# Performance work log

Measured on AMD Instinct MI355X. Metric: run time of the kernel, lower is better.

Reference implementation:

```python
import jax, jax.numpy as jnp
import numpy as np

NU, NI, DU, DI, E, B, T = 100000, 50000, 256, 256, 128, 8192, 24

def setup_inputs() -> dict:
    key = jax.random.key(0)
    ks = jax.random.split(key, 12)
    s = 0.05
    return {
        "nodes": jax.random.randint(ks[0], (B,), 0, NU),
        "neigh_idx": jax.random.randint(ks[1], (B, T), 0, NI),
        "u_weight": jax.random.normal(ks[2], (NU, DU), jnp.float32),
        "i_weight": jax.random.normal(ks[3], (NI, DI), jnp.float32),
        "uW": jax.random.normal(ks[4], (DU, E), jnp.float32) * s,
        "ub": jnp.zeros((E,), jnp.float32),
        "iW": jax.random.normal(ks[5], (DI, E), jnp.float32) * s,
        "ib": jnp.zeros((E,), jnp.float32),
        "aW1": jax.random.normal(ks[6], (2 * E, E), jnp.float32) * s,
        "ab1": jnp.zeros((E,), jnp.float32),
        "aW2": jax.random.normal(ks[7], (E, E), jnp.float32) * s,
        "ab2": jnp.zeros((E,), jnp.float32),
        "aW3": jax.random.normal(ks[8], (E, 1), jnp.float32) * s,
        "ab3": jnp.zeros((1,), jnp.float32),
    }


def reference(nodes, neigh_idx, u_weight, i_weight, uW, ub, iW, ib,
              aW1, ab1, aW2, ab2, aW3, ab3):
    # node features: u_layer(ufeature.weight[nodes])  -> [B, E]
    nodes_fea = u_weight[nodes] @ uW + ub
    # neighbor features: i_layer(ifeature.weight[interactions]) -> [B, T, E]
    neighs = i_weight[neigh_idx] @ iW + ib
    # attention MLP over cat(neigh_feat, node_feat.repeat) -> softmax over T
    x = jnp.concatenate(
        [neighs, jnp.broadcast_to(nodes_fea[:, None, :], neighs.shape)], axis=-1)
    h = jax.nn.relu(x @ aW1 + ab1)
    h = jax.nn.relu(h @ aW2 + ab2)
    logits = (h @ aW3 + ab3)[..., 0]            # [B, T]
    att = jax.nn.softmax(logits, axis=-1)       # softmax over neighbors (dim=0 per node)
    # attention-weighted aggregation: neighs_feature.T @ att_w  -> [B, E]
    agg = jnp.einsum('bt,bte->be', att, neighs)
    # scatter into embed_matrix rows of the batch nodes
    embed_matrix = jnp.zeros((NU, E), jnp.float32).at[nodes].set(agg)
    return nodes_fea, embed_matrix
```

## Files before the change

kernel.cpp:

```cpp
#include <hip/hip_runtime.h>
#include <math.h>

#define NU 100000
#define NI 50000
#define DK 256
#define EN 128
#define BB 8192
#define TT 24

typedef short short8 __attribute__((ext_vector_type(8)));
typedef float f32x4  __attribute__((ext_vector_type(4)));

#define WPACK_SHORTS 114688
#define WP_OFF     0
#define OWNER_OFF  229376
#define NTAB_OFF   629376
#define NPART_OFF  13429376

#define OFF_IWT   0
#define OFF_UWT   32768
#define OFF_AW1UT 65536
#define OFF_AW1LT 81920
#define OFF_AW2T  98304

#define NBLK_NEIGH 782
#define NBLK_NF    128
#define NBLK_PACK  448
#define GGA 4
#define ATTN_BLKS  (BB / GGA)

__device__ __forceinline__ unsigned short f2b(float x) {
    unsigned int u = __float_as_uint(x);
    u = (u + 0x7FFFu + ((u >> 16) & 1u)) >> 16;
    return (unsigned short)u;
}
__device__ __forceinline__ float b2f(unsigned short v) {
    return __uint_as_float(((unsigned int)v) << 16);
}
__device__ __forceinline__ unsigned int cvtpk_bf16(float lo, float hi) {
    unsigned int r;
    asm("v_cvt_pk_bf16_f32 %0, %1, %2" : "=v"(r) : "v"(lo), "v"(hi));
    return r;
}

#define MFMA(a, b, c) __builtin_amdgcn_mfma_f32_16x16x32_bf16((a), (b), (c), 0, 0, 0)
#define LDROW(buf, stride, row, k) \
    (*reinterpret_cast<const short8*>(reinterpret_cast<const char*>(buf) + (row) * (stride) + (k) * 2))

__global__ __launch_bounds__(256)
void prep_kernel(const int* __restrict__ nodes,
                 const float* __restrict__ uW, const float* __restrict__ iW,
                 const float* __restrict__ aW1, const float* __restrict__ aW2,
                 short* __restrict__ wp, int* __restrict__ owner)
{
    if (blockIdx.x < NBLK_PACK) {
        int i = blockIdx.x * 256 + threadIdx.x;
        float v;
        if (i < 32768)      { int j = i;         int n = j >> 8, k = j & 255; v = iW[k * EN + n]; }
        else if (i < 65536) { int j = i - 32768; int n = j >> 8, k = j & 255; v = uW[k * EN + n]; }
        else if (i < 81920) { int j = i - 65536; int n = j >> 7, k = j & 127; v = aW1[k * EN + n]; }
        else if (i < 98304) { int j = i - 81920; int n = j >> 7, k = j & 127; v = aW1[(128 + k) * EN + n]; }
        else                { int j = i - 98304; int n = j >> 7, k = j & 127; v = aW2[k * EN + n]; }
        wp[i] = (short)f2b(v);
    } else {
        int b = (blockIdx.x - NBLK_PACK) * 256 + threadIdx.x;
        if (b < BB) owner[nodes[b]] = -1;
    }
}

__global__ __launch_bounds__(256, 4)
void embed_kernel(const int* __restrict__ nodes,
                  const float* __restrict__ u_weight, const float* __restrict__ i_weight,
                  const float* __restrict__ ub, const float* __restrict__ ib,
                  const float* __restrict__ ab1,
                  const short* __restrict__ wp, int* __restrict__ owner,
                  short* __restrict__ ntab, float* __restrict__ out_nf,
                  float* __restrict__ npart, float* __restrict__ out_embed)
{
    __shared__ __align__(16) char smem[33792];
    __shared__ int sNd[64];

    const int tid = threadIdx.x;
    const int l = tid & 63, lr = l & 15, lq = l >> 4, n0 = (tid >> 6) * 32;
    const int kA = lq * 8, nc0 = n0 + lr, nc1 = n0 + 16 + lr;

    if (blockIdx.x < NBLK_NEIGH) {
        const int r0 = blockIdx.x * 64;
        const int nrows = (NI - r0 < 64) ? (NI - r0) : 64;

        for (int task = tid; task < 64 * 32; task += 256) {
            int row = task >> 5, c = task & 31;
            if (row < nrows) {
                const float* src = i_weight + (size_t)(r0 + row) * DK + c * 8;
                float4 f0 = *(const float4*)src;
                float4 f1 = *(const float4*)(src + 4);
                short8 o;
                o[0]=f2b(f0.x); o[1]=f2b(f0.y); o[2]=f2b(f0.z); o[3]=f2b(f0.w);
                o[4]=f2b(f1.x); o[5]=f2b(f1.y); o[6]=f2b(f1.z); o[7]=f2b(f1.w);
                *reinterpret_cast<short8*>(smem + row * 528 + c * 16) = o;
            }
        }
        __syncthreads();

        const short* iWt = wp + OFF_IWT;
        f32x4 acc[4][2];
        #pragma unroll
        for (int m = 0; m < 4; ++m) { acc[m][0] = {0.f,0.f,0.f,0.f}; acc[m][1] = {0.f,0.f,0.f,0.f}; }
        #pragma unroll
        for (int ks = 0; ks < 8; ++ks) {
            int k = ks * 32 + kA;
            short8 w0 = *reinterpret_cast<const short8*>(iWt + nc0 * DK + k);
            short8 w1 = *reinterpret_cast<const short8*>(iWt + nc1 * DK + k);
            #pragma unroll
            for (int m = 0; m < 4; ++m) {
                short8 a = LDROW(smem, 528, m * 16 + lr, k);
                acc[m][0] = MFMA(a, w0, acc[m][0]);
                acc[m][1] = MFMA(a, w1, acc[m][1]);
            }
        }
        __syncthreads();
        {
            float ib0 = ib[nc0], ib1 = ib[nc1];
            #pragma unroll
            for (int m = 0; m < 4; ++m)
                #pragma unroll
                for (int nt = 0; nt < 2; ++nt) {
                    int n = nt ? nc1 : nc0;
                    float bv = nt ? ib1 : ib0;
                    #pragma unroll
                    for (int r = 0; r < 4; ++r) {
                        int row = m * 16 + lq * 4 + r;
                        *reinterpret_cast<short*>(smem + row * 264 + n * 2)
                            = (short)f2b(acc[m][nt][r] + bv);
                    }
                }
        }
        __syncthreads();
        for (int g = tid; g < nrows * 16; g += 256) {
            int row = g >> 4, s = g & 15;
            short8 v = *reinterpret_cast<const short8*>(smem + row * 264 + s * 16);
            *reinterpret_cast<short8*>(ntab + (size_t)(r0 + row) * EN + s * 8) = v;
        }
    } else {
        const int bblk = blockIdx.x - NBLK_NEIGH;
        const int r0 = bblk * 64;
        {
            int bq = bblk * 256 + tid;
            if (bq < BB) atomicMax(&owner[nodes[bq]], bq);
        }
        if (tid < 64) sNd[tid] = nodes[r0 + tid];
        __syncthreads();

        for (int task = tid; task < 64 * 32; task += 256) {
            int row = task >> 5, c = task & 31;
            const float* src = u_weight + (size_t)sNd[row] * DK + c * 8;
            float4 f0 = *(const float4*)src;
            float4 f1 = *(const float4*)(src + 4);
            short8 o;
            o[0]=f2b(f0.x); o[1]=f2b(f0.y); o[2]=f2b(f0.z); o[3]=f2b(f0.w);
            o[4]=f2b(f1.x); o[5]=f2b(f1.y); o[6]=f2b(f1.z); o[7]=f2b(f1.w);
            *reinterpret_cast<short8*>(smem + row * 528 + c * 16) = o;
        }
        __syncthreads();

        const short* uWt   = wp + OFF_UWT;
        const short* aW1Lt = wp + OFF_AW1LT;

        f32x4 acc[4][2];
        #pragma unroll
        for (int m = 0; m < 4; ++m) { acc[m][0] = {0.f,0.f,0.f,0.f}; acc[m][1] = {0.f,0.f,0.f,0.f}; }
        #pragma unroll
        for (int ks = 0; ks < 8; ++ks) {
            int k = ks * 32 + kA;
            short8 w0 = *reinterpret_cast<const short8*>(uWt + nc0 * DK + k);
            short8 w1 = *reinterpret_cast<const short8*>(uWt + nc1 * DK + k);
            #pragma unroll
            for (int m = 0; m < 4; ++m) {
                short8 a = LDROW(smem, 528, m * 16 + lr, k);
                acc[m][0] = MFMA(a, w0, acc[m][0]);
                acc[m][1] = MFMA(a, w1, acc[m][1]);
            }
        }
        __syncthreads();
        {
            float b0v = ub[nc0], b1v = ub[nc1];
            #pragma unroll
            for (int m = 0; m < 4; ++m)
                #pragma unroll
                for (int nt = 0; nt < 2; ++nt) {
                    int n = nt ? nc1 : nc0;
                    float bv = nt ? b1v : b0v;
                    #pragma unroll
                    for (int r = 0; r < 4; ++r) {
                        int row = m * 16 + lq * 4 + r;
                        float v = acc[m][nt][r] + bv;
                        out_nf[(size_t)(r0 + row) * EN + n] = v;
                        *reinterpret_cast<short*>(smem + row * 272 + n * 2) = (short)f2b(v);
                    }
                }
        }
        __syncthreads();

        f32x4 ap[4][2];
        #pragma unroll
        for (int m = 0; m < 4; ++m) { ap[m][0] = {0.f,0.f,0.f,0.f}; ap[m][1] = {0.f,0.f,0.f,0.f}; }
        #pragma unroll
        for (int ks = 0; ks < 4; ++ks) {
            int k = ks * 32 + kA;
            short8 w0 = *reinterpret_cast<const short8*>(aW1Lt + nc0 * EN + k);
            short8 w1 = *reinterpret_cast<const short8*>(aW1Lt + nc1 * EN + k);
            #pragma unroll
            for (int m = 0; m < 4; ++m) {
                short8 a = LDROW(smem, 272, m * 16 + lr, k);
                ap[m][0] = MFMA(a, w0, ap[m][0]);
                ap[m][1] = MFMA(a, w1, ap[m][1]);
            }
        }
        {
            float b0v = ab1[nc0], b1v = ab1[nc1];
            #pragma unroll
            for (int m = 0; m < 4; ++m)
                #pragma unroll
                for (int nt = 0; nt < 2; ++nt) {
                    int n = nt ? nc1 : nc0;
                    float bv = nt ? b1v : b0v;
                    #pragma unroll
                    for (int r = 0; r < 4; ++r) {
                        int row = m * 16 + lq * 4 + r;
                        npart[(size_t)(r0 + row) * EN + n] = ap[m][nt][r] + bv;
                    }
                }
        }
    }

    {
        float4* embed4 = (float4*)out_embed;
        const int n16 = NU * EN / 4;
        const int gsz = (NBLK_NEIGH + NBLK_NF) * 256;
        float4 z = {0.f, 0.f, 0.f, 0.f};
        for (int i = blockIdx.x * 256 + tid; i < n16; i += gsz) embed4[i] = z;
    }
}

__global__ __launch_bounds__(256, 6)
void attn_kernel(const int* __restrict__ nodes, const int* __restrict__ neigh_idx,
                 const float* __restrict__ ab2, const float* __restrict__ aW3,
                 const float* __restrict__ ab3, const short* __restrict__ wp,
                 const short* __restrict__ ntab, const float* __restrict__ npart,
                 const int* __restrict__ owner, float* __restrict__ out_embed)
{
    __shared__ __align__(16) char sbuf[96 * 264];
    __shared__ float sLogP[4][96];

    const int tid = threadIdx.x;
    const int b0  = blockIdx.x * GGA;
    const int l   = tid & 63, w = tid >> 6;
    const int lr  = l & 15, lq = l >> 4;
    const int n0  = w * 32;
    const int kA  = lq * 8, nc0 = n0 + lr, nc1 = n0 + 16 + lr;

    short8 keep0, keep1, keep2, keep3, keep4, keep5;
    {
        const int s = l & 15, q = l >> 4;
        #pragma unroll
        for (int j = 0; j < 6; ++j) {
            int trow = j * 4 + q;
            int idx = neigh_idx[(b0 + w) * TT + trow];
            short8 v = *reinterpret_cast<const short8*>(ntab + (size_t)idx * EN + s * 8);
            switch (j) {
                case 0: keep0 = v; break; case 1: keep1 = v; break;
                case 2: keep2 = v; break; case 3: keep3 = v; break;
                case 4: keep4 = v; break; default: keep5 = v; break;
            }
            *reinterpret_cast<short8*>(sbuf + (w * 24 + trow) * 264 + s * 16) = v;
        }
    }
    __syncthreads();

    const short* aW1Ut = wp + OFF_AW1UT;
    const short* aW2t  = wp + OFF_AW2T;

    f32x4 acc[6][2];
    #pragma unroll
    for (int m = 0; m < 6; ++m) { acc[m][0] = {0.f,0.f,0.f,0.f}; acc[m][1] = {0.f,0.f,0.f,0.f}; }
    #pragma unroll
    for (int ks = 0; ks < 4; ++ks) {
        int k = ks * 32 + kA;
        short8 w0 = *reinterpret_cast<const short8*>(aW1Ut + nc0 * EN + k);
        short8 w1 = *reinterpret_cast<const short8*>(aW1Ut + nc1 * EN + k);
        #pragma unroll
        for (int m = 0; m < 6; ++m) {
            short8 a = LDROW(sbuf, 264, m * 16 + lr, k);
            acc[m][0] = MFMA(a, w0, acc[m][0]);
            acc[m][1] = MFMA(a, w1, acc[m][1]);
        }
    }
    __syncthreads();

    #pragma unroll
    for (int m = 0; m < 6; ++m) {
        int g = (m == 0) ? 0 : (m == 1) ? ((lq < 2) ? 0 : 1)
              : (m == 2) ? 1 : (m == 3) ? 2 : (m == 4) ? ((lq < 2) ? 2 : 3) : 3;
        #pragma unroll
        for (int nt = 0; nt < 2; ++nt) {
            int n = nt ? nc1 : nc0;
            float np = npart[(size_t)(b0 + g) * EN + n];
            float v0 = fmaxf(acc[m][nt][0] + np, 0.f);
            float v1 = fmaxf(acc[m][nt][1] + np, 0.f);
            float v2 = fmaxf(acc[m][nt][2] + np, 0.f);
            float v3 = fmaxf(acc[m][nt][3] + np, 0.f);
            unsigned int p01 = cvtpk_bf16(v0, v1);
            unsigned int p23 = cvtpk_bf16(v2, v3);
            char* base = sbuf + (m * 16 + lq * 4) * 264 + n * 2;
            *reinterpret_cast<short*>(base)       = (short)(p01 & 0xFFFF);
            *reinterpret_cast<short*>(base + 264) = (short)(p01 >> 16);
            *reinterpret_cast<short*>(base + 528) = (short)(p23 & 0xFFFF);
            *reinterpret_cast<short*>(base + 792) = (short)(p23 >> 16);
        }
    }
    __syncthreads();

    #pragma unroll
    for (int m = 0; m < 6; ++m) { acc[m][0] = {0.f,0.f,0.f,0.f}; acc[m][1] = {0.f,0.f,0.f,0.f}; }
    #pragma unroll
    for (int ks = 0; ks < 4; ++ks) {
        int k = ks * 32 + kA;
        short8 w0 = *reinterpret_cast<const short8*>(aW2t + nc0 * EN + k);
        short8 w1 = *reinterpret_cast<const short8*>(aW2t + nc1 * EN + k);
        #pragma unroll
        for (int m = 0; m < 6; ++m) {
            short8 a = LDROW(sbuf, 264, m * 16 + lr, k);
            acc[m][0] = MFMA(a, w0, acc[m][0]);
            acc[m][1] = MFMA(a, w1, acc[m][1]);
        }
    }
    {
        float b0v = ab2[nc0], b1v = ab2[nc1];
        float w3a = aW3[nc0], w3b = aW3[nc1];
        #pragma unroll
        for (int m = 0; m < 6; ++m) {
            float lp[4];
            #pragma unroll
            for (int r = 0; r < 4; ++r) {
                float v0 = fmaxf(acc[m][0][r] + b0v, 0.f);
                float v1 = fmaxf(acc[m][1][r] + b1v, 0.f);
                lp[r] = v0 * w3a + v1 * w3b;
            }
            #pragma unroll
            for (int r = 0; r < 4; ++r) {
                float v = lp[r];
                v += __shfl_xor(v, 1, 16);
                v += __shfl_xor(v, 2, 16);
                v += __shfl_xor(v, 4, 16);
                v += __shfl_xor(v, 8, 16);
                if (lr == 0) sLogP[w][m * 16 + lq * 4 + r] = v;
            }
        }
    }
    __syncthreads();

    float lg = -1e30f;
    if (l < TT)
        lg = sLogP[0][w * 24 + l] + sLogP[1][w * 24 + l]
           + sLogP[2][w * 24 + l] + sLogP[3][w * 24 + l] + ab3[0];
    float mx = lg;
    #pragma unroll
    for (int d = 32; d > 0; d >>= 1) mx = fmaxf(mx, __shfl_xor(mx, d, 64));
    float p = (l < TT) ? __expf(lg - mx) : 0.f;
    float s = p;
    #pragma unroll
    for (int d = 32; d > 0; d >>= 1) s += __shfl_xor(s, d, 64);
    float att = p / s;

    {
        float part[8] = {0.f,0.f,0.f,0.f,0.f,0.f,0.f,0.f};
        const int q = l >> 4;
        #pragma unroll
        for (int j = 0; j < 6; ++j) {
            float wt = __shfl(att, j * 4 + q, 64);
            short8 v = (j == 0) ? keep0 : (j == 1) ? keep1 : (j == 2) ? keep2
                     : (j == 3) ? keep3 : (j == 4) ? keep4 : keep5;
            #pragma unroll
            for (int e = 0; e < 8; ++e)
                part[e] += wt * b2f((unsigned short)v[e]);
        }
        #pragma unroll
        for (int e = 0; e < 8; ++e) {
            part[e] += __shfl_xor(part[e], 16, 64);
            part[e] += __shfl_xor(part[e], 32, 64);
        }
        int node = nodes[b0 + w];
        if (l < 16 && owner[node] == b0 + w) {
            float4 o0 = {part[0], part[1], part[2], part[3]};
            float4 o1 = {part[4], part[5], part[6], part[7]};
            float4* dst = reinterpret_cast<float4*>(out_embed + (size_t)node * EN + l * 8);
            dst[0] = o0;
            dst[1] = o1;
        }
    }
}

extern "C" void kernel_launch(void* const* d_in, const int* in_sizes, int n_in,
                              void* d_out, int out_size, void* d_ws, size_t ws_size,
                              hipStream_t stream) {
    const int*   nodes     = (const int*)d_in[0];
    const int*   neigh_idx = (const int*)d_in[1];
    const float* u_weight  = (const float*)d_in[2];
    const float* i_weight  = (const float*)d_in[3];
    const float* uW  = (const float*)d_in[4];
    const float* ub  = (const float*)d_in[5];
    const float* iW  = (const float*)d_in[6];
    const float* ib  = (const float*)d_in[7];
    const float* aW1 = (const float*)d_in[8];
    const float* ab1 = (const float*)d_in[9];
    const float* aW2 = (const float*)d_in[10];
    const float* ab2 = (const float*)d_in[11];
    const float* aW3 = (const float*)d_in[12];
    const float* ab3 = (const float*)d_in[13];

    float* out_nf    = (float*)d_out;
    float* out_embed = out_nf + (size_t)BB * EN;

    char*  ws    = (char*)d_ws;
    short* wpack = (short*)(ws + WP_OFF);
    int*   owner = (int*)(ws + OWNER_OFF);
    short* ntab  = (short*)(ws + NTAB_OFF);
    float* npart = (float*)(ws + NPART_OFF);

    prep_kernel<<<NBLK_PACK + 32, 256, 0, stream>>>(nodes, uW, iW, aW1, aW2, wpack, owner);
    embed_kernel<<<NBLK_NEIGH + NBLK_NF, 256, 0, stream>>>(
        nodes, u_weight, i_weight, ub, ib, ab1, wpack, owner, ntab, out_nf, npart, out_embed);
    attn_kernel<<<ATTN_BLKS, 256, 0, stream>>>(nodes, neigh_idx, ab2, aW3, ab3,
                                               wpack, ntab, npart, owner, out_embed);
}
```

Baseline: 84.80 us.

## Process two node groups per attention block, prefetching second group's neighbors

Each attention block now handles two groups of four nodes, so half as many blocks are launched. The second group's neighbor-row gather is issued into registers before the first group's MLP compute, hiding gather latency behind the MFMA work. In exchange, more registers are held live, the launch bound drops to 3 waves per SIMD, and the number of blocks halves, which may reduce latency hiding across waves.

```diff
diff --git a/kernel.cpp b/kernel.cpp
--- a/kernel.cpp
+++ b/kernel.cpp
@@ -27,7 +27,8 @@
 #define NBLK_NF    128
 #define NBLK_PACK  448
 #define GGA 4
-#define ATTN_BLKS  (BB / GGA)
+#define NGRP 2
+#define ATTN_BLKS (BB / (GGA * NGRP))
 
 __device__ __forceinline__ unsigned short f2b(float x) {
     unsigned int u = __float_as_uint(x);
@@ -242,44 +243,16 @@
     }
 }
 
-__global__ __launch_bounds__(256, 6)
-void attn_kernel(const int* __restrict__ nodes, const int* __restrict__ neigh_idx,
-                 const float* __restrict__ ab2, const float* __restrict__ aW3,
-                 const float* __restrict__ ab3, const short* __restrict__ wp,
-                 const short* __restrict__ ntab, const float* __restrict__ npart,
-                 const int* __restrict__ owner, float* __restrict__ out_embed)
+__device__ __forceinline__ void attn_compute(
+    int b0, int l, int w, int lr, int lq, int nc0, int nc1, int kA,
+    char* sbuf, float (*sLogP)[96],
+    short8 k0, short8 k1, short8 k2, short8 k3, short8 k4, short8 k5,
+    const float* __restrict__ npart, const float* __restrict__ ab2,
+    const float* __restrict__ aW3, const float* __restrict__ ab3,
+    const short* __restrict__ aW1Ut, const short* __restrict__ aW2t,
+    const int* __restrict__ nodes, const int* __restrict__ owner,
+    float* __restrict__ out_embed)
 {
-    __shared__ __align__(16) char sbuf[96 * 264];
-    __shared__ float sLogP[4][96];
-
-    const int tid = threadIdx.x;
-    const int b0  = blockIdx.x * GGA;
-    const int l   = tid & 63, w = tid >> 6;
-    const int lr  = l & 15, lq = l >> 4;
-    const int n0  = w * 32;
-    const int kA  = lq * 8, nc0 = n0 + lr, nc1 = n0 + 16 + lr;
-
-    short8 keep0, keep1, keep2, keep3, keep4, keep5;
-    {
-        const int s = l & 15, q = l >> 4;
-        #pragma unroll
-        for (int j = 0; j < 6; ++j) {
-            int trow = j * 4 + q;
-            int idx = neigh_idx[(b0 + w) * TT + trow];
-            short8 v = *reinterpret_cast<const short8*>(ntab + (size_t)idx * EN + s * 8);
-            switch (j) {
-                case 0: keep0 = v; break; case 1: keep1 = v; break;
-                case 2: keep2 = v; break; case 3: keep3 = v; break;
-                case 4: keep4 = v; break; default: keep5 = v; break;
-            }
-            *reinterpret_cast<short8*>(sbuf + (w * 24 + trow) * 264 + s * 16) = v;
-        }
-    }
-    __syncthreads();
-
-    const short* aW1Ut = wp + OFF_AW1UT;
-    const short* aW2t  = wp + OFF_AW2T;
-
     f32x4 acc[6][2];
     #pragma unroll
     for (int m = 0; m < 6; ++m) { acc[m][0] = {0.f,0.f,0.f,0.f}; acc[m][1] = {0.f,0.f,0.f,0.f}; }
@@ -311,7 +284,7 @@
             float v3 = fmaxf(acc[m][nt][3] + np, 0.f);
             unsigned int p01 = cvtpk_bf16(v0, v1);
             unsigned int p23 = cvtpk_bf16(v2, v3);
-            char* base = sbuf + (m * 16 + lq * 4) * 264 + n * 2;
+            char* base = sbuf + (m * 16 + lq * 4) * 264 + (nt ? nc1 : nc0) * 2;
             *reinterpret_cast<short*>(base)       = (short)(p01 & 0xFFFF);
             *reinterpret_cast<short*>(base + 264) = (short)(p01 >> 16);
             *reinterpret_cast<short*>(base + 528) = (short)(p23 & 0xFFFF);
@@ -378,8 +351,8 @@
         #pragma unroll
         for (int j = 0; j < 6; ++j) {
             float wt = __shfl(att, j * 4 + q, 64);
-            short8 v = (j == 0) ? keep0 : (j == 1) ? keep1 : (j == 2) ? keep2
-                     : (j == 3) ? keep3 : (j == 4) ? keep4 : keep5;
+            short8 v = (j == 0) ? k0 : (j == 1) ? k1 : (j == 2) ? k2
+                     : (j == 3) ? k3 : (j == 4) ? k4 : k5;
             #pragma unroll
             for (int e = 0; e < 8; ++e)
                 part[e] += wt * b2f((unsigned short)v[e]);
@@ -393,11 +366,78 @@
         if (l < 16 && owner[node] == b0 + w) {
             float4 o0 = {part[0], part[1], part[2], part[3]};
             float4 o1 = {part[4], part[5], part[6], part[7]};
-            float4* dst = reinterpret_cast<float4*>(out_embed + (size_t)node * EN + l * 8);
+            float4* dst = reinterpret_cast<float4*>(out_embed + (size_t)node * EN + (l & 15) * 8);
             dst[0] = o0;
             dst[1] = o1;
         }
     }
+}
+
+__global__ __launch_bounds__(256, 3)
+void attn_kernel(const int* __restrict__ nodes, const int* __restrict__ neigh_idx,
+                 const float* __restrict__ ab2, const float* __restrict__ aW3,
+                 const float* __restrict__ ab3, const short* __restrict__ wp,
+                 const short* __restrict__ ntab, const float* __restrict__ npart,
+                 const int* __restrict__ owner, float* __restrict__ out_embed)
+{
+    __shared__ __align__(16) char sbuf[96 * 264];
+    __shared__ float sLogP[4][96];
+
+    const int tid = threadIdx.x;
+    const int l   = tid & 63, w = tid >> 6;
+    const int lr  = l & 15, lq = l >> 4;
+    const int n0  = w * 32;
+    const int kA  = lq * 8, nc0 = n0 + lr, nc1 = n0 + 16 + lr;
+    const int s   = l & 15, q = l >> 4;
+
+    const short* aW1Ut = wp + OFF_AW1UT;
+    const short* aW2t  = wp + OFF_AW2T;
+
+    const int b0a = blockIdx.x * GGA;
+    const int b0b = (blockIdx.x + ATTN_BLKS) * GGA;
+
+#define GLOAD(dst, bb, j) { \
+        int idx_ = neigh_idx[((bb) + w) * TT + (j) * 4 + q]; \
+        dst = *reinterpret_cast<const short8*>(ntab + (size_t)idx_ * EN + s * 8); }
+
+    short8 k0, k1, k2, k3, k4, k5;
+    GLOAD(k0, b0a, 0) GLOAD(k1, b0a, 1) GLOAD(k2, b0a, 2)
+    GLOAD(k3, b0a, 3) GLOAD(k4, b0a, 4) GLOAD(k5, b0a, 5)
+    {
+        char* base = sbuf + (w * 24 + q) * 264 + s * 16;
+        *reinterpret_cast<short8*>(base)            = k0;
+        *reinterpret_cast<short8*>(base + 4 * 264)  = k1;
+        *reinterpret_cast<short8*>(base + 8 * 264)  = k2;
+        *reinterpret_cast<short8*>(base + 12 * 264) = k3;
+        *reinterpret_cast<short8*>(base + 16 * 264) = k4;
+        *reinterpret_cast<short8*>(base + 20 * 264) = k5;
+    }
+    __syncthreads();
+
+    short8 t0, t1, t2, t3, t4, t5;
+    GLOAD(t0, b0b, 0) GLOAD(t1, b0b, 1) GLOAD(t2, b0b, 2)
+    GLOAD(t3, b0b, 3) GLOAD(t4, b0b, 4) GLOAD(t5, b0b, 5)
+
+    attn_compute(b0a, l, w, lr, lq, nc0, nc1, kA, sbuf, sLogP,
+                 k0, k1, k2, k3, k4, k5,
+                 npart, ab2, aW3, ab3, aW1Ut, aW2t, nodes, owner, out_embed);
+    __syncthreads();
+
+    {
+        char* base = sbuf + (w * 24 + q) * 264 + s * 16;
+        *reinterpret_cast<short8*>(base)            = t0;
+        *reinterpret_cast<short8*>(base + 4 * 264)  = t1;
+        *reinterpret_cast<short8*>(base + 8 * 264)  = t2;
+        *reinterpret_cast<short8*>(base + 12 * 264) = t3;
+        *reinterpret_cast<short8*>(base + 16 * 264) = t4;
+        *reinterpret_cast<short8*>(base + 20 * 264) = t5;
+    }
+    __syncthreads();
+
+    attn_compute(b0b, l, w, lr, lq, nc0, nc1, kA, sbuf, sLogP,
+                 t0, t1, t2, t3, t4, t5,
+                 npart, ab2, aW3, ab3, aW1Ut, aW2t, nodes, owner, out_embed);
+#undef GLOAD
 }
 
 extern "C" void kernel_launch(void* const* d_in, const int* in_sizes, int n_in,
```

New measurement: 117.8 us. 1.39x slower.
